# Optimization experiments

Measured on AMD Instinct MI355X. Metric: run time of the kernel, lower is better.

## Reference

```python
import jax, jax.numpy as jnp
import numpy as np

GROUP = 64

def dequant(W_q, scale, zero):
    # W_q: [out, in] int, scale/zero: [out, in//GROUP]
    out, din = W_q.shape
    g = din // GROUP
    Wq = W_q.reshape(out, g, GROUP).astype(scale.dtype)
    W = (Wq - zero[:, :, None]) * scale[:, :, None]
    return W.reshape(out, din)

def setup_inputs() -> dict:
    key = jax.random.key(0)
    ks = jax.random.split(key, 10)
    T, H, F = 512, 4096, 14336
    return {
        "hidden_states": jax.random.normal(ks[0], (T, H), jnp.float32),
        "W1_q": jax.random.randint(ks[1], (F, H), 0, 16, jnp.int32),
        "w1_scale": jax.random.uniform(ks[2], (F, H // GROUP), jnp.float32, 1e-3, 0.02),
        "w1_zero": jax.random.uniform(ks[3], (F, H // GROUP), jnp.float32, 6.0, 9.0),
        "W3_q": jax.random.randint(ks[4], (F, H), 0, 16, jnp.int32),
        "w3_scale": jax.random.uniform(ks[5], (F, H // GROUP), jnp.float32, 1e-3, 0.02),
        "w3_zero": jax.random.uniform(ks[6], (F, H // GROUP), jnp.float32, 6.0, 9.0),
        "W2_q": jax.random.randint(ks[7], (H, F), 0, 16, jnp.int32),
        "w2_scale": jax.random.uniform(ks[8], (H, F // GROUP), jnp.float32, 1e-3, 0.02),
        "w2_zero": jax.random.uniform(ks[9], (H, F // GROUP), jnp.float32, 6.0, 9.0),
    }

def reference(hidden_states, W1_q, w1_scale, w1_zero, W3_q, w3_scale, w3_zero, W2_q, w2_scale, w2_zero):
    W1 = dequant(W1_q, w1_scale, w1_zero)  # [F, H]
    W3 = dequant(W3_q, w3_scale, w3_zero)  # [F, H]
    W2 = dequant(W2_q, w2_scale, w2_zero)  # [H, F]
    g = jax.nn.silu(hidden_states @ W1.T) * (hidden_states @ W3.T)  # [T, F]
    return g @ W2.T  # [T, H]
```

## Files before the change

### kernel.cpp

```cpp
#include <hip/hip_runtime.h>
#include <hip/hip_bf16.h>

#define T_DIM 512
#define H_DIM 4096
#define F_DIM 14336
#define KSEG  8

typedef __attribute__((ext_vector_type(8))) short bf16x8;
typedef __attribute__((ext_vector_type(4))) float f32x4;

__device__ __forceinline__ unsigned short f2bf(float f) {
    union { __hip_bfloat16 h; unsigned short u; } cv;
    cv.h = __float2bfloat16(f);
    return cv.u;
}

__device__ __forceinline__ void dq16(int4 qv, float s, float z, unsigned short* dst) {
    float nzs = -z * s;
    ushort4 o;
    o.x = f2bf(fmaf((float)qv.x, s, nzs));
    o.y = f2bf(fmaf((float)qv.y, s, nzs));
    o.z = f2bf(fmaf((float)qv.z, s, nzs));
    o.w = f2bf(fmaf((float)qv.w, s, nzs));
    *(ushort4*)dst = o;
}

__device__ __forceinline__ void gload16(const void* g, void* l) {
    __builtin_amdgcn_global_load_lds(
        (const __attribute__((address_space(1))) void*)(unsigned long long)(uintptr_t)g,
        (__attribute__((address_space(3))) void*)(uintptr_t)l, 16, 0, 0);
}

__global__ __launch_bounds__(256) void zero_out(float4* __restrict__ out) {
    out[blockIdx.x * 256 + threadIdx.x] = make_float4(0.f, 0.f, 0.f, 0.f);
}

__global__ __launch_bounds__(256) void cvt_x(const float* __restrict__ X,
                                             unsigned short* __restrict__ Xb) {
    int i = (blockIdx.x * 256 + threadIdx.x) * 4;
    float4 v = *(const float4*)&X[i];
    ushort4 o;
    o.x = f2bf(v.x); o.y = f2bf(v.y); o.z = f2bf(v.z); o.w = f2bf(v.w);
    *(ushort4*)&Xb[i] = o;
}

__global__ __launch_bounds__(256, 2)
void gate_up_kernel(const unsigned short* __restrict__ Xb,
                    const int* __restrict__ W1q, const float* __restrict__ sc1,
                    const float* __restrict__ zp1,
                    const int* __restrict__ W3q, const float* __restrict__ sc3,
                    const float* __restrict__ zp3,
                    unsigned short* __restrict__ G)
{
    constexpr int LK = 72;
    constexpr int XB = 128 * 64 * 2;
    constexpr int WB = 64 * LK * 2;
    constexpr int BUFB = XB + 2 * WB;
    __shared__ __align__(16) char smem[2 * BUFB];
    float* sEx = (float*)smem;

    const int t = threadIdx.x, wave = t >> 6, lane = t & 63;
    const int r = lane & 15, q = lane >> 4;
    const int mh  = (wave & 1) * 64;
    const int mat = wave >> 1;
    const int rs  = r & 7;

    const int b = blockIdx.x;
    const int xcd = b & 7, lb = b >> 3;
    const int m0 = (lb & 3) * 128;
    const int n0 = (xcd * 28 + (lb >> 2)) * 64;
    const int SG = H_DIM / 64;

    const int wrow = t >> 4, wc = (t & 15) * 4;

    const int lrow = lane >> 3;
    const int lc   = (lane & 7) ^ lrow;
    const unsigned short* xsrc =
        Xb + (size_t)(m0 + wave * 32 + lrow) * H_DIM + lc * 8;

    int4 pW1[4], pW3[4];

    {
        #pragma unroll
        for (int i = 0; i < 4; ++i) {
            size_t off = (size_t)(n0 + wrow + 16 * i) * H_DIM + wc;
            pW1[i] = *(const int4*)&W1q[off];
            pW3[i] = *(const int4*)&W3q[off];
        }
        #pragma unroll
        for (int j = 0; j < 4; ++j)
            gload16(xsrc + (size_t)j * 8 * H_DIM, smem + (wave * 4 + j) * 1024);
        unsigned short* sW1 = (unsigned short*)(smem + XB);
        unsigned short* sW3 = (unsigned short*)(smem + XB + WB);
        #pragma unroll
        for (int i = 0; i < 4; ++i) {
            int row = wrow + 16 * i;
            int sidx = (n0 + row) * SG;
            dq16(pW1[i], sc1[sidx], zp1[sidx], &sW1[row * LK + wc]);
            dq16(pW3[i], sc3[sidx], zp3[sidx], &sW3[row * LK + wc]);
        }
    }
    __syncthreads();

    f32x4 acc[4][4];
    #pragma unroll
    for (int a = 0; a < 4; ++a)
        #pragma unroll
        for (int c = 0; c < 4; ++c) acc[a][c] = (f32x4){0.f, 0.f, 0.f, 0.f};

    constexpr int NIT = H_DIM / 64;
    #pragma unroll 2
    for (int it = 0; it < NIT; ++it) {
        const char* cb = smem + (it & 1) * BUFB;
        char* nb = smem + ((it + 1) & 1) * BUFB;
        const int kn = (it + 1) * 64;

        if (it + 1 < NIT) {
            #pragma unroll
            for (int i = 0; i < 4; ++i) {
                size_t off = (size_t)(n0 + wrow + 16 * i) * H_DIM + kn + wc;
                pW1[i] = *(const int4*)&W1q[off];
                pW3[i] = *(const int4*)&W3q[off];
            }
            #pragma unroll
            for (int j = 0; j < 4; ++j)
                gload16(xsrc + (size_t)j * 8 * H_DIM + kn,
                        nb + (wave * 4 + j) * 1024);
        }

        const unsigned short* sX = (const unsigned short*)cb;
        const unsigned short* sB = (const unsigned short*)(cb + XB + mat * WB);
        #pragma unroll
        for (int kh = 0; kh < 2; ++kh) {
            const int kb = kh * 32 + q * 8;
            const int xc = (kh * 4 + q) ^ rs;
            bf16x8 av[4], bv[4];
            #pragma unroll
            for (int im = 0; im < 4; ++im)
                av[im] = *(const bf16x8*)&sX[(mh + im * 16 + r) * 64 + xc * 8];
            #pragma unroll
            for (int j = 0; j < 4; ++j)
                bv[j] = *(const bf16x8*)&sB[(j * 16 + r) * LK + kb];
            #pragma unroll
            for (int im = 0; im < 4; ++im)
                #pragma unroll
                for (int j = 0; j < 4; ++j)
                    acc[im][j] = __builtin_amdgcn_mfma_f32_16x16x32_bf16(av[im], bv[j], acc[im][j], 0, 0, 0);
        }

        if (it + 1 < NIT) {
            unsigned short* nW1 = (unsigned short*)(nb + XB);
            unsigned short* nW3 = (unsigned short*)(nb + XB + WB);
            const int gidx = it + 1;
            #pragma unroll
            for (int i = 0; i < 4; ++i) {
                int row = wrow + 16 * i;
                int sidx = (n0 + row) * SG + gidx;
                dq16(pW1[i], sc1[sidx], zp1[sidx], &nW1[row * LK + wc]);
                dq16(pW3[i], sc3[sidx], zp3[sidx], &nW3[row * LK + wc]);
            }
            __syncthreads();
        }
    }

    if (mat == 1) {
        #pragma unroll
        for (int im = 0; im < 4; ++im)
            #pragma unroll
            for (int j = 0; j < 4; ++j)
                #pragma unroll
                for (int reg = 0; reg < 4; ++reg)
                    sEx[(mh + im * 16 + q * 4 + reg) * 65 + j * 16 + r] = acc[im][j][reg];
    }
    __syncthreads();
    if (mat == 0) {
        #pragma unroll
        for (int im = 0; im < 4; ++im)
            #pragma unroll
            for (int j = 0; j < 4; ++j)
                #pragma unroll
                for (int reg = 0; reg < 4; ++reg) {
                    int ml = mh + im * 16 + q * 4 + reg;
                    int nl = j * 16 + r;
                    float g1 = acc[im][j][reg];
                    float g3 = sEx[ml * 65 + nl];
                    float val = g1 / (1.f + __expf(-g1)) * g3;
                    G[(size_t)(m0 + ml) * F_DIM + n0 + nl] = f2bf(val);
                }
    }
}

__global__ __launch_bounds__(256, 2)
void down_kernel(const unsigned short* __restrict__ G,
                 const int* __restrict__ W2q, const float* __restrict__ sc2,
                 const float* __restrict__ zp2,
                 float* __restrict__ Out)
{
    constexpr int LK = 72;
    constexpr int AB = 128 * 64 * 2;
    constexpr int WB = 128 * LK * 2;
    constexpr int BUFB = AB + WB;
    __shared__ __align__(16) char smem[2 * BUFB];

    const int t = threadIdx.x, wave = t >> 6, lane = t & 63;
    const int r = lane & 15, q = lane >> 4;
    const int wm = (wave & 1) * 64, wn = (wave >> 1) * 64;
    const int rs = r & 7;

    const int b = blockIdx.x;
    const int xcd = b & 7, lb = b >> 3;
    const int m0 = (lb & 3) * 128;
    const int pair = xcd * 32 + (lb >> 2);
    const int n0 = (pair >> 3) * 128;
    const int kbeg = (pair & 7) * (F_DIM / KSEG);
    const int SG = F_DIM / 64;

    const int wrow = t >> 4, wc = (t & 15) * 4;

    const int lrow = lane >> 3;
    const int lc   = (lane & 7) ^ lrow;
    const unsigned short* asrc =
        G + (size_t)(m0 + wave * 32 + lrow) * F_DIM + kbeg + lc * 8;

    int4 pW[8];

    {
        #pragma unroll
        for (int i = 0; i < 8; ++i)
            pW[i] = *(const int4*)&W2q[(size_t)(n0 + wrow + 16 * i) * F_DIM + kbeg + wc];
        #pragma unroll
        for (int j = 0; j < 4; ++j)
            gload16(asrc + (size_t)j * 8 * F_DIM, smem + (wave * 4 + j) * 1024);
        unsigned short* sW = (unsigned short*)(smem + AB);
        const int gidx = kbeg >> 6;
        #pragma unroll
        for (int i = 0; i < 8; ++i) {
            int row = wrow + 16 * i;
            int sidx = (n0 + row) * SG + gidx;
            dq16(pW[i], sc2[sidx], zp2[sidx], &sW[row * LK + wc]);
        }
    }
    __syncthreads();

    f32x4 acc[4][4];
    #pragma unroll
    for (int a = 0; a < 4; ++a)
        #pragma unroll
        for (int c = 0; c < 4; ++c) acc[a][c] = (f32x4){0.f, 0.f, 0.f, 0.f};

    constexpr int NIT = (F_DIM / KSEG) / 64;
    #pragma unroll 2
    for (int it = 0; it < NIT; ++it) {
        const char* cb = smem + (it & 1) * BUFB;
        char* nb = smem + ((it + 1) & 1) * BUFB;
        const int kn = kbeg + (it + 1) * 64;

        if (it + 1 < NIT) {
            #pragma unroll
            for (int i = 0; i < 8; ++i)
                pW[i] = *(const int4*)&W2q[(size_t)(n0 + wrow + 16 * i) * F_DIM + kn + wc];
            #pragma unroll
            for (int j = 0; j < 4; ++j)
                gload16(asrc + (size_t)j * 8 * F_DIM + (it + 1) * 64,
                        nb + (wave * 4 + j) * 1024);
        }

        const unsigned short* sA = (const unsigned short*)cb;
        const unsigned short* sW = (const unsigned short*)(cb + AB);
        #pragma unroll
        for (int kh = 0; kh < 2; ++kh) {
            const int kb = kh * 32 + q * 8;
            const int xc = (kh * 4 + q) ^ rs;
            bf16x8 av[4], bv[4];
            #pragma unroll
            for (int im = 0; im < 4; ++im)
                av[im] = *(const bf16x8*)&sA[(wm + im * 16 + r) * 64 + xc * 8];
            #pragma unroll
            for (int j = 0; j < 4; ++j)
                bv[j] = *(const bf16x8*)&sW[(wn + j * 16 + r) * LK + kb];
            #pragma unroll
            for (int im = 0; im < 4; ++im)
                #pragma unroll
                for (int j = 0; j < 4; ++j)
                    acc[im][j] = __builtin_amdgcn_mfma_f32_16x16x32_bf16(av[im], bv[j], acc[im][j], 0, 0, 0);
        }

        if (it + 1 < NIT) {
            unsigned short* nW = (unsigned short*)(nb + AB);
            const int gidx = kn >> 6;
            #pragma unroll
            for (int i = 0; i < 8; ++i) {
                int row = wrow + 16 * i;
                int sidx = (n0 + row) * SG + gidx;
                dq16(pW[i], sc2[sidx], zp2[sidx], &nW[row * LK + wc]);
            }
            __syncthreads();
        }
    }

    #pragma unroll
    for (int im = 0; im < 4; ++im)
        #pragma unroll
        for (int j = 0; j < 4; ++j)
            #pragma unroll
            for (int reg = 0; reg < 4; ++reg) {
                int m = m0 + wm + im * 16 + q * 4 + reg;
                int h = n0 + wn + j * 16 + r;
                atomicAdd(&Out[(size_t)m * H_DIM + h], acc[im][j][reg]);
            }
}

extern "C" void kernel_launch(void* const* d_in, const int* in_sizes, int n_in,
                              void* d_out, int out_size, void* d_ws, size_t ws_size,
                              hipStream_t stream) {
    const float* X   = (const float*)d_in[0];
    const int*   W1q = (const int*)d_in[1];
    const float* s1  = (const float*)d_in[2];
    const float* z1  = (const float*)d_in[3];
    const int*   W3q = (const int*)d_in[4];
    const float* s3  = (const float*)d_in[5];
    const float* z3  = (const float*)d_in[6];
    const int*   W2q = (const int*)d_in[7];
    const float* s2  = (const float*)d_in[8];
    const float* z2  = (const float*)d_in[9];
    float* Out = (float*)d_out;

    unsigned short* Xb = (unsigned short*)d_ws;
    unsigned short* G  = (unsigned short*)((char*)d_ws + (4 << 20));

    zero_out<<<2048, 256, 0, stream>>>((float4*)Out);
    cvt_x<<<2048, 256, 0, stream>>>(X, Xb);
    gate_up_kernel<<<896, 256, 0, stream>>>(Xb, W1q, s1, z1, W3q, s3, z3, G);
    down_kernel<<<1024, 256, 0, stream>>>(G, W2q, s2, z2, Out);
}
```

Before: 940.1 us.

## Prefetch weights two stages ahead and replace atomic split-K with partial-sum reduction

Both GEMM kernels now issue the next-next weight tile's global loads right after dequantizing the current one, so load latency overlaps a full MFMA stage. The down projection halves its split-K factor from 8 to 4 and writes plain stores into per-segment partial buffers. A separate reduce kernel then sums the buffers into the output, replacing the zeroing kernel and the float atomics. The down kernel now launches only 512 blocks, which may underfill the GPU, and adds a 32MB partial-buffer write and read plus one extra launch.

```diff
diff --git a/kernel.cpp b/kernel.cpp
--- a/kernel.cpp
+++ b/kernel.cpp
@@ -4,7 +4,7 @@
 #define T_DIM 512
 #define H_DIM 4096
 #define F_DIM 14336
-#define KSEG  8
+#define KSEG  4
 
 typedef __attribute__((ext_vector_type(8))) short bf16x8;
 typedef __attribute__((ext_vector_type(4))) float f32x4;
@@ -31,10 +31,6 @@
         (__attribute__((address_space(3))) void*)(uintptr_t)l, 16, 0, 0);
 }
 
-__global__ __launch_bounds__(256) void zero_out(float4* __restrict__ out) {
-    out[blockIdx.x * 256 + threadIdx.x] = make_float4(0.f, 0.f, 0.f, 0.f);
-}
-
 __global__ __launch_bounds__(256) void cvt_x(const float* __restrict__ X,
                                              unsigned short* __restrict__ Xb) {
     int i = (blockIdx.x * 256 + threadIdx.x) * 4;
@@ -42,6 +38,15 @@
     ushort4 o;
     o.x = f2bf(v.x); o.y = f2bf(v.y); o.z = f2bf(v.z); o.w = f2bf(v.w);
     *(ushort4*)&Xb[i] = o;
+}
+
+__global__ __launch_bounds__(256) void reduce_out(const float4* __restrict__ P,
+                                                  float4* __restrict__ out) {
+    constexpr size_t S = (size_t)T_DIM * H_DIM / 4;
+    size_t i = (size_t)blockIdx.x * 256 + threadIdx.x;
+    float4 a = P[i], b = P[i + S], c = P[i + 2 * S], d = P[i + 3 * S];
+    out[i] = make_float4(a.x + b.x + c.x + d.x, a.y + b.y + c.y + d.y,
+                         a.z + b.z + c.z + d.z, a.w + b.w + c.w + d.w);
 }
 
 __global__ __launch_bounds__(256, 2)
@@ -82,14 +87,14 @@
 
     {
         #pragma unroll
+        for (int j = 0; j < 4; ++j)
+            gload16(xsrc + (size_t)j * 8 * H_DIM, smem + (wave * 4 + j) * 1024);
+        #pragma unroll
         for (int i = 0; i < 4; ++i) {
             size_t off = (size_t)(n0 + wrow + 16 * i) * H_DIM + wc;
             pW1[i] = *(const int4*)&W1q[off];
             pW3[i] = *(const int4*)&W3q[off];
         }
-        #pragma unroll
-        for (int j = 0; j < 4; ++j)
-            gload16(xsrc + (size_t)j * 8 * H_DIM, smem + (wave * 4 + j) * 1024);
         unsigned short* sW1 = (unsigned short*)(smem + XB);
         unsigned short* sW3 = (unsigned short*)(smem + XB + WB);
         #pragma unroll
@@ -99,6 +104,12 @@
             dq16(pW1[i], sc1[sidx], zp1[sidx], &sW1[row * LK + wc]);
             dq16(pW3[i], sc3[sidx], zp3[sidx], &sW3[row * LK + wc]);
         }
+        #pragma unroll
+        for (int i = 0; i < 4; ++i) {
+            size_t off = (size_t)(n0 + wrow + 16 * i) * H_DIM + 64 + wc;
+            pW1[i] = *(const int4*)&W1q[off];
+            pW3[i] = *(const int4*)&W3q[off];
+        }
     }
     __syncthreads();
 
@@ -113,15 +124,9 @@
     for (int it = 0; it < NIT; ++it) {
         const char* cb = smem + (it & 1) * BUFB;
         char* nb = smem + ((it + 1) & 1) * BUFB;
-        const int kn = (it + 1) * 64;
 
         if (it + 1 < NIT) {
-            #pragma unroll
-            for (int i = 0; i < 4; ++i) {
-                size_t off = (size_t)(n0 + wrow + 16 * i) * H_DIM + kn + wc;
-                pW1[i] = *(const int4*)&W1q[off];
-                pW3[i] = *(const int4*)&W3q[off];
-            }
+            const int kn = (it + 1) * 64;
             #pragma unroll
             for (int j = 0; j < 4; ++j)
                 gload16(xsrc + (size_t)j * 8 * H_DIM + kn,
@@ -158,6 +163,15 @@
                 int sidx = (n0 + row) * SG + gidx;
                 dq16(pW1[i], sc1[sidx], zp1[sidx], &nW1[row * LK + wc]);
                 dq16(pW3[i], sc3[sidx], zp3[sidx], &nW3[row * LK + wc]);
+            }
+            if (it + 2 < NIT) {
+                const int kf = (it + 2) * 64;
+                #pragma unroll
+                for (int i = 0; i < 4; ++i) {
+                    size_t off = (size_t)(n0 + wrow + 16 * i) * H_DIM + kf + wc;
+                    pW1[i] = *(const int4*)&W1q[off];
+                    pW3[i] = *(const int4*)&W3q[off];
+                }
             }
             __syncthreads();
         }
@@ -194,7 +208,7 @@
 void down_kernel(const unsigned short* __restrict__ G,
                  const int* __restrict__ W2q, const float* __restrict__ sc2,
                  const float* __restrict__ zp2,
-                 float* __restrict__ Out)
+                 float* __restrict__ Parts)
 {
     constexpr int LK = 72;
     constexpr int AB = 128 * 64 * 2;
@@ -210,9 +224,10 @@
     const int b = blockIdx.x;
     const int xcd = b & 7, lb = b >> 3;
     const int m0 = (lb & 3) * 128;
-    const int pair = xcd * 32 + (lb >> 2);
-    const int n0 = (pair >> 3) * 128;
-    const int kbeg = (pair & 7) * (F_DIM / KSEG);
+    const int pair = xcd * 16 + (lb >> 2);
+    const int n0 = (pair >> 2) * 128;
+    const int ks = pair & 3;
+    const int kbeg = ks * (F_DIM / KSEG);
     const int SG = F_DIM / 64;
 
     const int wrow = t >> 4, wc = (t & 15) * 4;
@@ -226,11 +241,11 @@
 
     {
         #pragma unroll
+        for (int j = 0; j < 4; ++j)
+            gload16(asrc + (size_t)j * 8 * F_DIM, smem + (wave * 4 + j) * 1024);
+        #pragma unroll
         for (int i = 0; i < 8; ++i)
             pW[i] = *(const int4*)&W2q[(size_t)(n0 + wrow + 16 * i) * F_DIM + kbeg + wc];
-        #pragma unroll
-        for (int j = 0; j < 4; ++j)
-            gload16(asrc + (size_t)j * 8 * F_DIM, smem + (wave * 4 + j) * 1024);
         unsigned short* sW = (unsigned short*)(smem + AB);
         const int gidx = kbeg >> 6;
         #pragma unroll
@@ -239,6 +254,9 @@
             int sidx = (n0 + row) * SG + gidx;
             dq16(pW[i], sc2[sidx], zp2[sidx], &sW[row * LK + wc]);
         }
+        #pragma unroll
+        for (int i = 0; i < 8; ++i)
+            pW[i] = *(const int4*)&W2q[(size_t)(n0 + wrow + 16 * i) * F_DIM + kbeg + 64 + wc];
     }
     __syncthreads();
 
@@ -253,15 +271,12 @@
     for (int it = 0; it < NIT; ++it) {
         const char* cb = smem + (it & 1) * BUFB;
         char* nb = smem + ((it + 1) & 1) * BUFB;
-        const int kn = kbeg + (it + 1) * 64;
 
         if (it + 1 < NIT) {
-            #pragma unroll
-            for (int i = 0; i < 8; ++i)
-                pW[i] = *(const int4*)&W2q[(size_t)(n0 + wrow + 16 * i) * F_DIM + kn + wc];
-            #pragma unroll
-            for (int j = 0; j < 4; ++j)
-                gload16(asrc + (size_t)j * 8 * F_DIM + (it + 1) * 64,
+            const int kn = (it + 1) * 64;
+            #pragma unroll
+            for (int j = 0; j < 4; ++j)
+                gload16(asrc + (size_t)j * 8 * F_DIM + kn,
                         nb + (wave * 4 + j) * 1024);
         }
 
@@ -287,17 +302,24 @@
 
         if (it + 1 < NIT) {
             unsigned short* nW = (unsigned short*)(nb + AB);
-            const int gidx = kn >> 6;
+            const int gidx = (kbeg + (it + 1) * 64) >> 6;
             #pragma unroll
             for (int i = 0; i < 8; ++i) {
                 int row = wrow + 16 * i;
                 int sidx = (n0 + row) * SG + gidx;
                 dq16(pW[i], sc2[sidx], zp2[sidx], &nW[row * LK + wc]);
             }
+            if (it + 2 < NIT) {
+                const int kf = kbeg + (it + 2) * 64;
+                #pragma unroll
+                for (int i = 0; i < 8; ++i)
+                    pW[i] = *(const int4*)&W2q[(size_t)(n0 + wrow + 16 * i) * F_DIM + kf + wc];
+            }
             __syncthreads();
         }
     }
 
+    float* P = Parts + (size_t)ks * T_DIM * H_DIM;
     #pragma unroll
     for (int im = 0; im < 4; ++im)
         #pragma unroll
@@ -306,7 +328,7 @@
             for (int reg = 0; reg < 4; ++reg) {
                 int m = m0 + wm + im * 16 + q * 4 + reg;
                 int h = n0 + wn + j * 16 + r;
-                atomicAdd(&Out[(size_t)m * H_DIM + h], acc[im][j][reg]);
+                P[(size_t)m * H_DIM + h] = acc[im][j][reg];
             }
 }
 
@@ -327,9 +349,10 @@
 
     unsigned short* Xb = (unsigned short*)d_ws;
     unsigned short* G  = (unsigned short*)((char*)d_ws + (4 << 20));
-
-    zero_out<<<2048, 256, 0, stream>>>((float4*)Out);
+    float* Parts       = (float*)((char*)d_ws + (20 << 20));
+
     cvt_x<<<2048, 256, 0, stream>>>(X, Xb);
     gate_up_kernel<<<896, 256, 0, stream>>>(Xb, W1q, s1, z1, W3q, s3, z3, G);
-    down_kernel<<<1024, 256, 0, stream>>>(G, W2q, s2, z2, Out);
-}
+    down_kernel<<<512, 256, 0, stream>>>(G, W2q, s2, z2, Parts);
+    reduce_out<<<2048, 256, 0, stream>>>((const float4*)Parts, (float4*)Out);
+}
```

Result: faster. 834.9 us (-11.2%).
